# Performance work log

Hardware: AMD Instinct MI355X
Metric: run time of the kernel (lower is better)

Reference implementation:

```python
import jax, jax.numpy as jnp
import numpy as np

MAXDISP = 48
GROUP = 8
EPS = 1e-5


def setup_inputs() -> dict:
    key = jax.random.key(0)
    k1, k2 = jax.random.split(key)
    x = jax.random.normal(k1, (2, 64, 96, 320), dtype=jnp.float32)
    y = jax.random.normal(k2, (2, 64, 96, 320), dtype=jnp.float32)
    return {"x": x, "y": y}


def reference(x, y):
    # Faithful translation of CostVolume.forward.
    # torch's unfold over left-zero-padded y at kernel position d picks
    # y_pad[..., j + d]; per-window L2 norm over channels reduces to a
    # per-pixel channel norm (padded zeros normalize to zero), so we
    # normalize once and gather shifted columns.
    D = MAXDISP + 1
    b, c, h, w = x.shape
    cpg = c // GROUP
    xg = x.reshape(b, GROUP, cpg, h, w)
    yg = y.reshape(b, GROUP, cpg, h, w)
    xn = xg / (jnp.linalg.norm(xg, axis=2, keepdims=True) + EPS)
    yn = yg / (jnp.linalg.norm(yg, axis=2, keepdims=True) + EPS)
    # left zero-pad width dim by MAXDISP (padded zeros stay zero after norm)
    y_pad = jnp.pad(yn, ((0, 0), (0, 0), (0, 0), (0, 0), (MAXDISP, 0)))
    # after torch.flip on the disparity axis, disparity k compares x[:, j]
    # with y[:, j - k]  ->  padded index j + MAXDISP - k
    idx = jnp.arange(w)[None, :] + MAXDISP - jnp.arange(D)[:, None]  # [D, w]
    y_shift = y_pad[..., idx]  # [b, g, cpg, h, D, w]
    cost = jnp.sum(jnp.abs(xn[:, :, :, :, None, :] - y_shift), axis=2)  # [b,g,h,D,w]
    return jnp.transpose(cost, (0, 1, 3, 2, 4))  # [b, group, D, h, w]
```

## Files before the change

kernel.cpp:

```cpp
#include <hip/hip_runtime.h>


#define HH    96
#define WW    320
#define HW    (HH * WW)
#define NDISP 49
#define EPSN  1e-5f

__global__ __launch_bounds__(WW, 4) void cost_volume_kernel(
    const float* __restrict__ x, const float* __restrict__ y,
    float* __restrict__ out)
{
    __shared__ float xn_s[8][WW];
    __shared__ float yn_s[8][WW];

    const int t   = threadIdx.x;
    const int blk = blockIdx.x;
    const int h   = blk % HH;
    const int bg  = blk / HH;

    const size_t base = (size_t)bg * 8 * HW + (size_t)h * WW;

    {
        float xv[8], yv[8];
        float xs = 0.f, ys = 0.f;
#pragma unroll
        for (int cc = 0; cc < 8; ++cc) {
            float xi = x[base + (size_t)cc * HW + t];
            float yi = y[base + (size_t)cc * HW + t];
            xv[cc] = xi; yv[cc] = yi;
            xs += xi * xi;
            ys += yi * yi;
        }
        const float xinv = 1.f / (sqrtf(xs) + EPSN);
        const float yinv = 1.f / (sqrtf(ys) + EPSN);
#pragma unroll
        for (int cc = 0; cc < 8; ++cc) {
            xn_s[cc][t] = xv[cc] * xinv;
            yn_s[cc][t] = yv[cc] * yinv;
        }
    }
    __syncthreads();

    const int w  = t >> 6;
    const int l  = t & 63;
    const int q  = w * 16 + (l & 15);
    const int dc = l >> 4;
    const int Q  = 4 * q;

    float4 xq[8];
#pragma unroll
    for (int cc = 0; cc < 8; ++cc)
        xq[cc] = *(const float4*)&xn_s[cc][Q];

    float4 sA = make_float4(0.f, 0.f, 0.f, 0.f);
#pragma unroll
    for (int cc = 0; cc < 8; ++cc) {
        sA.x += fabsf(xq[cc].x);  sA.y += fabsf(xq[cc].y);
        sA.z += fabsf(xq[cc].z);  sA.w += fabsf(xq[cc].w);
    }

    float* outp = out + (size_t)bg * (NDISP * HW) + (size_t)h * WW + Q;

#pragma unroll
    for (int gi = 0; gi < 3; ++gi) {
        const int g = 3 * dc + gi;
        int wq0 = q - g - 1; if (wq0 < 0) wq0 = 0;
        int wq1 = q - g;     if (wq1 < 0) wq1 = 0;
        const int a0 = 4 * wq0;
        const int a1 = 4 * wq1;

        float acc[4][4];
#pragma unroll
        for (int e = 0; e < 4; ++e)
#pragma unroll
            for (int k = 0; k < 4; ++k) acc[e][k] = 0.f;

#pragma unroll
        for (int cc = 0; cc < 8; ++cc) {
            const float4 wa = *(const float4*)&yn_s[cc][a0];
            const float4 wb = *(const float4*)&yn_s[cc][a1];
            const float win[8] = { wa.x, wa.y, wa.z, wa.w,
                                   wb.x, wb.y, wb.z, wb.w };
            const float4 xc = xq[cc];
#pragma unroll
            for (int e = 0; e < 4; ++e) {
                acc[e][0] += fabsf(xc.x - win[4 - e]);
                acc[e][1] += fabsf(xc.y - win[5 - e]);
                acc[e][2] += fabsf(xc.z - win[6 - e]);
                acc[e][3] += fabsf(xc.w - win[7 - e]);
            }
        }

#pragma unroll
        for (int e = 0; e < 4; ++e) {
            const int d = 4 * g + e;
            float4 rr;
            rr.x = (Q + 0 < d) ? sA.x : acc[e][0];
            rr.y = (Q + 1 < d) ? sA.y : acc[e][1];
            rr.z = (Q + 2 < d) ? sA.z : acc[e][2];
            rr.w = (Q + 3 < d) ? sA.w : acc[e][3];
            *(float4*)&outp[(size_t)d * HW] = rr;
        }
    }

    {
        int wq = q - 12; if (wq < 0) wq = 0;
        const int a = 4 * wq;
        float4 acc = make_float4(0.f, 0.f, 0.f, 0.f);
#pragma unroll
        for (int cc = 0; cc < 8; ++cc) {
            const float4 wv = *(const float4*)&yn_s[cc][a];
            acc.x += fabsf(xq[cc].x - wv.x);
            acc.y += fabsf(xq[cc].y - wv.y);
            acc.z += fabsf(xq[cc].z - wv.z);
            acc.w += fabsf(xq[cc].w - wv.w);
        }
        float4 rr;
        rr.x = (Q + 0 < 48) ? sA.x : acc.x;
        rr.y = (Q + 1 < 48) ? sA.y : acc.y;
        rr.z = (Q + 2 < 48) ? sA.z : acc.z;
        rr.w = (Q + 3 < 48) ? sA.w : acc.w;
        if (dc == 0)
            *(float4*)&outp[(size_t)48 * HW] = rr;
    }
}

extern "C" void kernel_launch(void* const* d_in, const int* in_sizes, int n_in,
                              void* d_out, int out_size, void* d_ws, size_t ws_size,
                              hipStream_t stream) {
    const float* x = (const float*)d_in[0];
    const float* y = (const float*)d_in[1];
    float* out = (float*)d_out;
    dim3 grid(16 * HH);
    dim3 block(WW);
    cost_volume_kernel<<<grid, block, 0, stream>>>(x, y, out);
}
```

Before: 131.5 us.

## Interchange loops to share y windows across disparity groups in one channel pass

The channel loop now sits outside the three disparity groups, and all 52 accumulators live in registers at once. Adjacent groups share y-window float4 loads, so each channel needs 5 LDS loads instead of 2 per group plus the extra disparity-48 pass, and x is read from LDS per channel rather than kept as 8 float4 registers. This cuts LDS traffic but raises register pressure, which could hurt occupancy under the launch bounds of 4 blocks of 320 threads.

```diff
diff --git a/kernel.cpp b/kernel.cpp
--- a/kernel.cpp
+++ b/kernel.cpp
@@ -42,85 +42,86 @@
     }
     __syncthreads();
 
-    const int w  = t >> 6;
     const int l  = t & 63;
-    const int q  = w * 16 + (l & 15);
+    const int q  = (t >> 6) * 16 + (l & 15);
     const int dc = l >> 4;
     const int Q  = 4 * q;
+    const int W  = q - 3 * dc - 3;
 
-    float4 xq[8];
+    int a[4];
 #pragma unroll
-    for (int cc = 0; cc < 8; ++cc)
-        xq[cc] = *(const float4*)&xn_s[cc][Q];
+    for (int k = 0; k < 4; ++k) {
+        int wq = W + k; if (wq < 0) wq = 0;
+        a[k] = 4 * wq;
+    }
+    int wq48 = q - 12; if (wq48 < 0) wq48 = 0;
+    const int a48 = 4 * wq48;
 
-    float4 sA = make_float4(0.f, 0.f, 0.f, 0.f);
+    float acc[3][4][4];
+#pragma unroll
+    for (int gi = 0; gi < 3; ++gi)
+#pragma unroll
+        for (int e = 0; e < 4; ++e)
+#pragma unroll
+            for (int k = 0; k < 4; ++k) acc[gi][e][k] = 0.f;
+    float acc48[4] = {0.f, 0.f, 0.f, 0.f};
+    float sA[4]    = {0.f, 0.f, 0.f, 0.f};
+
 #pragma unroll
     for (int cc = 0; cc < 8; ++cc) {
-        sA.x += fabsf(xq[cc].x);  sA.y += fabsf(xq[cc].y);
-        sA.z += fabsf(xq[cc].z);  sA.w += fabsf(xq[cc].w);
+        const float* row = yn_s[cc];
+        const float4 w0 = *(const float4*)&row[a[0]];
+        const float4 w1 = *(const float4*)&row[a[1]];
+        const float4 w2 = *(const float4*)&row[a[2]];
+        const float4 w3 = *(const float4*)&row[a[3]];
+        const float4 w4 = *(const float4*)&row[a48];
+        const float4 xc = *(const float4*)&xn_s[cc][Q];
+
+        const float wf[16] = { w0.x, w0.y, w0.z, w0.w,
+                               w1.x, w1.y, w1.z, w1.w,
+                               w2.x, w2.y, w2.z, w2.w,
+                               w3.x, w3.y, w3.z, w3.w };
+        const float xk[4] = { xc.x, xc.y, xc.z, xc.w };
+
+#pragma unroll
+        for (int k = 0; k < 4; ++k) sA[k] += fabsf(xk[k]);
+
+#pragma unroll
+        for (int gi = 0; gi < 3; ++gi) {
+            const int b0 = (2 - gi) * 4;
+#pragma unroll
+            for (int e = 0; e < 4; ++e)
+#pragma unroll
+                for (int k = 0; k < 4; ++k)
+                    acc[gi][e][k] += fabsf(xk[k] - wf[b0 + k + 4 - e]);
+        }
+        acc48[0] += fabsf(xk[0] - w4.x);
+        acc48[1] += fabsf(xk[1] - w4.y);
+        acc48[2] += fabsf(xk[2] - w4.z);
+        acc48[3] += fabsf(xk[3] - w4.w);
     }
 
     float* outp = out + (size_t)bg * (NDISP * HW) + (size_t)h * WW + Q;
 
 #pragma unroll
     for (int gi = 0; gi < 3; ++gi) {
-        const int g = 3 * dc + gi;
-        int wq0 = q - g - 1; if (wq0 < 0) wq0 = 0;
-        int wq1 = q - g;     if (wq1 < 0) wq1 = 0;
-        const int a0 = 4 * wq0;
-        const int a1 = 4 * wq1;
-
-        float acc[4][4];
-#pragma unroll
-        for (int e = 0; e < 4; ++e)
-#pragma unroll
-            for (int k = 0; k < 4; ++k) acc[e][k] = 0.f;
-
-#pragma unroll
-        for (int cc = 0; cc < 8; ++cc) {
-            const float4 wa = *(const float4*)&yn_s[cc][a0];
-            const float4 wb = *(const float4*)&yn_s[cc][a1];
-            const float win[8] = { wa.x, wa.y, wa.z, wa.w,
-                                   wb.x, wb.y, wb.z, wb.w };
-            const float4 xc = xq[cc];
-#pragma unroll
-            for (int e = 0; e < 4; ++e) {
-                acc[e][0] += fabsf(xc.x - win[4 - e]);
-                acc[e][1] += fabsf(xc.y - win[5 - e]);
-                acc[e][2] += fabsf(xc.z - win[6 - e]);
-                acc[e][3] += fabsf(xc.w - win[7 - e]);
-            }
-        }
-
 #pragma unroll
         for (int e = 0; e < 4; ++e) {
-            const int d = 4 * g + e;
+            const int d = 4 * (3 * dc + gi) + e;
             float4 rr;
-            rr.x = (Q + 0 < d) ? sA.x : acc[e][0];
-            rr.y = (Q + 1 < d) ? sA.y : acc[e][1];
-            rr.z = (Q + 2 < d) ? sA.z : acc[e][2];
-            rr.w = (Q + 3 < d) ? sA.w : acc[e][3];
+            rr.x = (Q + 0 < d) ? sA[0] : acc[gi][e][0];
+            rr.y = (Q + 1 < d) ? sA[1] : acc[gi][e][1];
+            rr.z = (Q + 2 < d) ? sA[2] : acc[gi][e][2];
+            rr.w = (Q + 3 < d) ? sA[3] : acc[gi][e][3];
             *(float4*)&outp[(size_t)d * HW] = rr;
         }
     }
-
     {
-        int wq = q - 12; if (wq < 0) wq = 0;
-        const int a = 4 * wq;
-        float4 acc = make_float4(0.f, 0.f, 0.f, 0.f);
-#pragma unroll
-        for (int cc = 0; cc < 8; ++cc) {
-            const float4 wv = *(const float4*)&yn_s[cc][a];
-            acc.x += fabsf(xq[cc].x - wv.x);
-            acc.y += fabsf(xq[cc].y - wv.y);
-            acc.z += fabsf(xq[cc].z - wv.z);
-            acc.w += fabsf(xq[cc].w - wv.w);
-        }
         float4 rr;
-        rr.x = (Q + 0 < 48) ? sA.x : acc.x;
-        rr.y = (Q + 1 < 48) ? sA.y : acc.y;
-        rr.z = (Q + 2 < 48) ? sA.z : acc.z;
-        rr.w = (Q + 3 < 48) ? sA.w : acc.w;
+        rr.x = (Q + 0 < 48) ? sA[0] : acc48[0];
+        rr.y = (Q + 1 < 48) ? sA[1] : acc48[1];
+        rr.z = (Q + 2 < 48) ? sA[2] : acc48[2];
+        rr.w = (Q + 3 < 48) ? sA[3] : acc48[3];
         if (dc == 0)
             *(float4*)&outp[(size_t)48 * HW] = rr;
     }
```

Measured after the change: 155.0 us. 17.9% more time.
